# Performance work log

Hardware: AMD Instinct MI355X
Metric: run time of the kernel (lower is better)

## Reference

```python
import jax, jax.numpy as jnp
import numpy as np
from jax import lax

K = 3
PAD = 1
DIL = 1
BN_EPS = 1e-5


def setup_inputs() -> dict:
    key = jax.random.key(0)
    ks = jax.random.split(key, 7)
    B, C, O, H, W = 4, 64, 64, 128, 128
    x = jax.random.normal(ks[0], (B, C, H, W), jnp.float32)
    # offset conv params (zero-init in the module; small random here to exercise bilinear sampling)
    w_off = jax.random.normal(ks[1], (2 * K * K, C, K, K), jnp.float32) * 0.01
    b_off = jax.random.normal(ks[2], (2 * K * K,), jnp.float32) * 0.01
    # deformable conv params
    w_dcn = jax.random.normal(ks[3], (O, C, K, K), jnp.float32) / np.sqrt(C * K * K).astype(np.float32)
    b_dcn = jax.random.normal(ks[4], (O,), jnp.float32) * 0.01
    # BatchNorm affine params
    gamma = 1.0 + 0.1 * jax.random.normal(ks[5], (O,), jnp.float32)
    beta = 0.1 * jax.random.normal(ks[6], (O,), jnp.float32)
    return dict(x=x, w_off=w_off, b_off=b_off, w_dcn=w_dcn, b_dcn=b_dcn, gamma=gamma, beta=beta)


def _conv2d(x, w):
    return lax.conv_general_dilated(
        x, w, window_strides=(1, 1), padding=[(PAD, PAD), (PAD, PAD)],
        rhs_dilation=(DIL, DIL), dimension_numbers=('NCHW', 'OIHW', 'NCHW'))


def _gather(x, iy, ix):
    # x: [B,C,H,W]; iy/ix: [B,K2,H,W] int32 (already clipped in-range)
    B, C, H, W = x.shape
    idx = (iy * W + ix).reshape(B, -1)          # [B, K2*H*W]
    xf = x.reshape(B, C, H * W)
    v = jax.vmap(lambda xb, ib: xb[:, ib])(xf, idx)  # [B, C, K2*H*W]
    return v.reshape(B, C, iy.shape[1], H, W)


def _deform_sample(x, offset):
    # torchvision DeformConv2d v1: offsets are (dy, dx) pairs per kernel tap, zero-padding bilinear.
    B, C, H, W = x.shape
    K2 = K * K
    off = offset.reshape(B, K2, 2, H, W)
    ky = jnp.repeat(jnp.arange(K), K)   # tap row index, k = ky*K + kx
    kx = jnp.tile(jnp.arange(K), K)
    py = off[:, :, 0] + (ky * DIL - PAD)[None, :, None, None] + jnp.arange(H)[None, None, :, None]
    px = off[:, :, 1] + (kx * DIL - PAD)[None, :, None, None] + jnp.arange(W)[None, None, None, :]
    y0 = jnp.floor(py)
    x0 = jnp.floor(px)
    wy = py - y0
    wx = px - x0
    y0i = y0.astype(jnp.int32)
    x0i = x0.astype(jnp.int32)
    acc = jnp.zeros((B, C, K2, H, W), x.dtype)
    for dy, dx in ((0, 0), (0, 1), (1, 0), (1, 1)):
        iy = y0i + dy
        ix = x0i + dx
        wgt = (wy if dy else 1.0 - wy) * (wx if dx else 1.0 - wx)
        valid = (iy >= 0) & (iy < H) & (ix >= 0) & (ix < W)
        v = _gather(x, jnp.clip(iy, 0, H - 1), jnp.clip(ix, 0, W - 1))
        acc = acc + v * (wgt * valid.astype(x.dtype))[:, None]
    return acc  # [B, C, K2, H, W]


def reference(x, w_off, b_off, w_dcn, b_dcn, gamma, beta):
    offset = _conv2d(x, w_off) + b_off[None, :, None, None]
    patches = _deform_sample(x, offset)                     # [B,C,K2,H,W]
    O = w_dcn.shape[0]
    out = jnp.einsum('bckhw,ock->bohw', patches, w_dcn.reshape(O, -1, K * K))
    out = out + b_dcn[None, :, None, None]
    # BatchNorm2d in training mode: biased batch statistics over (B,H,W)
    mean = out.mean(axis=(0, 2, 3), keepdims=True)
    var = out.var(axis=(0, 2, 3), keepdims=True)
    out = (out - mean) * lax.rsqrt(var + BN_EPS)
    out = out * gamma[None, :, None, None] + beta[None, :, None, None]
    return jax.nn.relu(out)
```

## Files before the change

kernel.cpp:

```cpp
#include <hip/hip_runtime.h>

#define HW   16384
#define WID  128
#define HEI  128
#define CIN  64
#define OCH  64

typedef __attribute__((ext_vector_type(8))) short bf16x8;
typedef __attribute__((ext_vector_type(4))) short bf16x4;
typedef __attribute__((ext_vector_type(4))) float f32x4;

__device__ __forceinline__ unsigned short f2bf(float f) {
    unsigned u = __float_as_uint(f);
    u += 0x7FFF + ((u >> 16) & 1);
    return (unsigned short)(u >> 16);
}
__device__ __forceinline__ float bf2f(short s) {
    return __uint_as_float(((unsigned)(unsigned short)s) << 16);
}

__global__ __launch_bounds__(256) void kprep(const float* __restrict__ x,
                                             const float* __restrict__ wdcn,
                                             const float* __restrict__ woff,
                                             unsigned short* __restrict__ xt,
                                             unsigned short* __restrict__ wpack,
                                             unsigned short* __restrict__ woffpack) {
    int blk = blockIdx.x;
    if (blk < 256) {
        int gp = blk * 256 + threadIdx.x;
        int b = gp >> 14;
        int hw = gp & (HW - 1);
        const float* xb = x + (size_t)b * CIN * HW + hw;
        unsigned short* o = xt + ((size_t)gp << 6);
#pragma unroll
        for (int c8 = 0; c8 < 8; c8++) {
            bf16x8 v;
#pragma unroll
            for (int j = 0; j < 8; j++)
                v[j] = (short)f2bf(xb[(size_t)(c8 * 8 + j) * HW]);
            *(bf16x8*)(o + c8 * 8) = v;
        }
    } else {
        int t = (blk - 256) * 256 + threadIdx.x;
        if (t < 36864) {
            int j  = t & 7;
            int l  = (t >> 3) & 63;
            int nt = (t >> 9) & 3;
            int s  = t >> 11;
            int k  = s * 32 + (l >> 4) * 8 + j;
            int o  = nt * 16 + (l & 15);
            int tap = k >> 6, c = k & 63;
            wpack[t] = f2bf(wdcn[o * 576 + c * 9 + tap]);
        } else {
            int u  = t - 36864;
            int j  = u & 7;
            int l  = (u >> 3) & 63;
            int nt = (u >> 9) & 1;
            int s  = u >> 10;
            int k  = s * 32 + (l >> 4) * 8 + j;
            int o  = nt * 16 + (l & 15);
            int tap = k >> 6, c = k & 63;
            float v = (o < 18) ? woff[o * 576 + c * 9 + tap] : 0.f;
            woffpack[u] = f2bf(v);
        }
    }
}

__global__ __launch_bounds__(256, 4) void kdcn(const unsigned short* __restrict__ xt,
                                               const unsigned short* __restrict__ wpack,
                                               const unsigned short* __restrict__ woffpack,
                                               const float* __restrict__ boff,
                                               const float* __restrict__ bdcn,
                                               unsigned short* __restrict__ convb,
                                               float* __restrict__ part) {
    __shared__ __align__(16) unsigned char smem[39168];

    int tid = threadIdx.x;
    int lane = tid & 63, wave = tid >> 6;
    int lr = lane & 15, hi = lane >> 4;

    int pixg = blockIdx.x * 32;
    int b = pixg >> 14;
    int hwb = pixg & (HW - 1);
    int h = hwb >> 7;
    int w0 = hwb & (WID - 1);

    {
        int g = lane >> 3, sub = lane & 7;
        int px = wave * 8 + g;
        int w = w0 + px;
        const unsigned char* xtb =
            (const unsigned char*)xt + (((size_t)b * HW) << 7) + sub * 16;
        unsigned char* prow = smem + px * 1152;
        unsigned swz = (unsigned)((px & 7) << 4);
#pragma unroll
        for (int tap = 0; tap < 9; tap++) {
            int sy = h + tap / 3 - 1;
            int sx = w + tap % 3 - 1;
            bool ok = ((unsigned)sy < HEI) && ((unsigned)sx < WID);
            bf16x8 v = {0, 0, 0, 0, 0, 0, 0, 0};
            if (ok) v = *(const bf16x8*)(xtb + ((sy * WID + sx) << 7));
            *(bf16x8*)(prow + ((unsigned)(tap * 128 + sub * 16) ^ swz)) = v;
        }
    }
    __syncthreads();

    {
        int mw = wave & 1, nw = wave >> 1;
        int oc = nw * 16 + lr;
        float ob = (oc < 18) ? boff[oc] : 0.f;
        f32x4 oacc = {ob, ob, ob, ob};
        unsigned swzr = (unsigned)((lr & 7) << 4);
        const unsigned short* wop = woffpack + (size_t)(nw * 64 + lane) * 8;
        int arow = (mw * 16 + lr) * 1152;
#pragma unroll
        for (int s = 0; s < 18; s++) {
            unsigned inblk = (unsigned)((s >> 1) * 128)
                           + (((unsigned)((s & 1) * 64 + hi * 16)) ^ swzr);
            bf16x8 a  = *(const bf16x8*)(smem + arow + inblk);
            bf16x8 wf = *(const bf16x8*)(wop + (size_t)s * 1024);
            oacc = __builtin_amdgcn_mfma_f32_16x16x32_bf16(a, wf, oacc, 0, 0, 0);
        }
        float* offLds = (float*)(smem + 36864);
        if (oc < 18) {
#pragma unroll
            for (int r = 0; r < 4; r++)
                offLds[(mw * 16 + hi * 4 + r) * 18 + oc] = oacc[r];
        }
    }

    bf16x8 bfrag[18];
    const unsigned short* wp = wpack + (size_t)(wave * 64 + lane) * 8;
#pragma unroll
    for (int s = 0; s < 18; s++)
        bfrag[s] = *(const bf16x8*)(wp + (size_t)s * 2048);
    float bias = bdcn[wave * 16 + lr];
    __syncthreads();

    {
        int g = lane >> 3, sub = lane & 7;
        int px = wave * 8 + g;
        int w = w0 + px;
        const unsigned char* xtb =
            (const unsigned char*)xt + (((size_t)b * HW) << 7) + sub * 16;
        unsigned char* prow = smem + px * 1152;
        unsigned swz = (unsigned)((px & 7) << 4);
        const float* offL = (const float*)(smem + 36864) + px * 18;
#pragma unroll
        for (int tap = 0; tap < 9; tap++) {
            float dy = offL[tap * 2];
            float dx = offL[tap * 2 + 1];
            float py  = dy + (float)(h + tap / 3 - 1);
            float pxf = dx + (float)(w + tap % 3 - 1);
            float y0f = floorf(py), x0f = floorf(pxf);
            float wy = py - y0f, wx = pxf - x0f;
            int y0 = (int)y0f, x0 = (int)x0f;
            float wy0 = ((unsigned)y0       < HEI) ? 1.f - wy : 0.f;
            float wy1 = ((unsigned)(y0 + 1) < HEI) ? wy       : 0.f;
            float wx0 = ((unsigned)x0       < WID) ? 1.f - wx : 0.f;
            float wx1 = ((unsigned)(x0 + 1) < WID) ? wx       : 0.f;
            int yc0 = min(max(y0, 0),     HEI - 1) * WID;
            int yc1 = min(max(y0 + 1, 0), HEI - 1) * WID;
            int xc0 = min(max(x0, 0),     WID - 1);
            int xc1 = min(max(x0 + 1, 0), WID - 1);
            float w00 = wy0 * wx0, w01 = wy0 * wx1;
            float w10 = wy1 * wx0, w11 = wy1 * wx1;
            bf16x8 c00 = *(const bf16x8*)(xtb + ((yc0 + xc0) << 7));
            bf16x8 c01 = *(const bf16x8*)(xtb + ((yc0 + xc1) << 7));
            bf16x8 c10 = *(const bf16x8*)(xtb + ((yc1 + xc0) << 7));
            bf16x8 c11 = *(const bf16x8*)(xtb + ((yc1 + xc1) << 7));
            bf16x8 v;
#pragma unroll
            for (int j = 0; j < 8; j++) {
                float sv = w00 * bf2f(c00[j]) + w01 * bf2f(c01[j])
                         + w10 * bf2f(c10[j]) + w11 * bf2f(c11[j]);
                v[j] = (short)f2bf(sv);
            }
            *(bf16x8*)(prow + ((unsigned)(tap * 128 + sub * 16) ^ swz)) = v;
        }
    }
    __syncthreads();

    f32x4 acc0 = {bias, bias, bias, bias};
    f32x4 acc1 = acc0;
    unsigned swzr = (unsigned)((lr & 7) << 4);
#pragma unroll
    for (int s = 0; s < 18; s++) {
        unsigned inblk = (unsigned)((s >> 1) * 128)
                       + (((unsigned)((s & 1) * 64 + hi * 16)) ^ swzr);
        bf16x8 a0 = *(const bf16x8*)(smem + lr * 1152 + inblk);
        bf16x8 a1 = *(const bf16x8*)(smem + (16 + lr) * 1152 + inblk);
        acc0 = __builtin_amdgcn_mfma_f32_16x16x32_bf16(a0, bfrag[s], acc0, 0, 0, 0);
        acc1 = __builtin_amdgcn_mfma_f32_16x16x32_bf16(a1, bfrag[s], acc1, 0, 0, 0);
    }

    {
        int o = wave * 16 + lr;
        unsigned short* cb = convb + ((size_t)b * OCH + o) * HW + hwb + hi * 4;
        bf16x4 v0, v1;
#pragma unroll
        for (int r = 0; r < 4; r++) { v0[r] = (short)f2bf(acc0[r]);
                                      v1[r] = (short)f2bf(acc1[r]); }
        *(bf16x4*)cb        = v0;
        *(bf16x4*)(cb + 16) = v1;
    }

    {
        float s  = acc0[0] + acc0[1] + acc0[2] + acc0[3]
                 + acc1[0] + acc1[1] + acc1[2] + acc1[3];
        float s2 = acc0[0]*acc0[0] + acc0[1]*acc0[1] + acc0[2]*acc0[2] + acc0[3]*acc0[3]
                 + acc1[0]*acc1[0] + acc1[1]*acc1[1] + acc1[2]*acc1[2] + acc1[3]*acc1[3];
        s  += __shfl_xor(s, 16);  s2 += __shfl_xor(s2, 16);
        s  += __shfl_xor(s, 32);  s2 += __shfl_xor(s2, 32);
        if (hi == 0) {
            int c = wave * 16 + lr;
            part[(size_t)c * 2048 + blockIdx.x]        = s;
            part[(size_t)(64 + c) * 2048 + blockIdx.x] = s2;
        }
    }
}

__global__ __launch_bounds__(256) void kred(const float* __restrict__ part,
                                            float* __restrict__ stats) {
    int row = blockIdx.x;
    int tid = threadIdx.x;
    const float* p = part + (size_t)row * 2048;
    float s = 0.f;
#pragma unroll
    for (int i = 0; i < 8; i++) s += p[tid + i * 256];
#pragma unroll
    for (int d = 1; d < 64; d <<= 1) s += __shfl_xor(s, d);
    __shared__ float red[4];
    if ((tid & 63) == 0) red[tid >> 6] = s;
    __syncthreads();
    if (tid == 0) stats[row] = red[0] + red[1] + red[2] + red[3];
}

__global__ __launch_bounds__(256) void kapply(const unsigned short* __restrict__ convb,
                                              float* __restrict__ out,
                                              const float* __restrict__ stats,
                                              const float* __restrict__ gamma,
                                              const float* __restrict__ beta) {
    int t = blockIdx.x * 256 + threadIdx.x;
    int c = (t >> 12) & 63;
    float mean = stats[c] * (1.f / 65536.f);
    float var  = stats[64 + c] * (1.f / 65536.f) - mean * mean;
    float rstd = rsqrtf(var + 1e-5f);
    float sc = rstd * gamma[c];
    float sh = beta[c] - mean * sc;
    bf16x4 v = *(const bf16x4*)(convb + (size_t)t * 4);
    float4 r;
    r.x = fmaxf(bf2f(v[0]) * sc + sh, 0.f);
    r.y = fmaxf(bf2f(v[1]) * sc + sh, 0.f);
    r.z = fmaxf(bf2f(v[2]) * sc + sh, 0.f);
    r.w = fmaxf(bf2f(v[3]) * sc + sh, 0.f);
    ((float4*)out)[t] = r;
}

extern "C" void kernel_launch(void* const* d_in, const int* in_sizes, int n_in,
                              void* d_out, int out_size, void* d_ws, size_t ws_size,
                              hipStream_t stream) {
    const float* x     = (const float*)d_in[0];
    const float* woff  = (const float*)d_in[1];
    const float* boff  = (const float*)d_in[2];
    const float* wdcn  = (const float*)d_in[3];
    const float* bdcn  = (const float*)d_in[4];
    const float* gamma = (const float*)d_in[5];
    const float* beta  = (const float*)d_in[6];
    float* out = (float*)d_out;

    unsigned char* ws = (unsigned char*)d_ws;
    unsigned short* xt       = (unsigned short*)ws;
    unsigned short* wpack    = (unsigned short*)(ws + 8388608);
    unsigned short* woffpack = (unsigned short*)(ws + 8462336);
    float*          part     = (float*)(ws + 8499200);
    float*          stats    = (float*)(ws + 9547776);
    unsigned short* convb    = (unsigned short*)(ws + 9548288);

    hipLaunchKernelGGL(kprep,  dim3(472),  dim3(256), 0, stream,
                       x, wdcn, woff, xt, wpack, woffpack);
    hipLaunchKernelGGL(kdcn,   dim3(2048), dim3(256), 0, stream,
                       xt, wpack, woffpack, boff, bdcn, convb, part);
    hipLaunchKernelGGL(kred,   dim3(128),  dim3(256), 0, stream, part, stats);
    hipLaunchKernelGGL(kapply, dim3(4096), dim3(256), 0, stream,
                       convb, out, stats, gamma, beta);
}
```

Before: 56.62 us.

## Restructure deformable conv kernel so each wave independently owns 16 pixels

Each wave now processes 16 pixels on its own. A fragments are loaded straight from global memory into registers, so the shared-memory im2col staging and the block-wide barriers are gone. Each wave computes its own offset conv over two output tiles and all four DCN output-channel tiles, and streams B weights from global (L2) memory per step instead of holding them in registers. Per-wave partial sums double, so the reduction kernel reads 4096 entries per row. This trades LDS traffic and synchronisation for more global/L2 weight loads and less reuse of B fragments across pixels.

```diff
diff --git a/kernel.cpp b/kernel.cpp
--- a/kernel.cpp
+++ b/kernel.cpp
@@ -66,156 +66,135 @@
     }
 }
 
-__global__ __launch_bounds__(256, 4) void kdcn(const unsigned short* __restrict__ xt,
-                                               const unsigned short* __restrict__ wpack,
-                                               const unsigned short* __restrict__ woffpack,
-                                               const float* __restrict__ boff,
-                                               const float* __restrict__ bdcn,
-                                               unsigned short* __restrict__ convb,
-                                               float* __restrict__ part) {
-    __shared__ __align__(16) unsigned char smem[39168];
+__global__ __launch_bounds__(256) void kdcn(const unsigned short* __restrict__ xt,
+                                            const unsigned short* __restrict__ wpack,
+                                            const unsigned short* __restrict__ woffpack,
+                                            const float* __restrict__ boff,
+                                            const float* __restrict__ bdcn,
+                                            unsigned short* __restrict__ convb,
+                                            float* __restrict__ part) {
+    __shared__ float offLds[4][288];
 
     int tid = threadIdx.x;
     int lane = tid & 63, wave = tid >> 6;
     int lr = lane & 15, hi = lane >> 4;
 
-    int pixg = blockIdx.x * 32;
+    int gw = blockIdx.x * 4 + wave;
+    int pixg = gw << 4;
     int b = pixg >> 14;
     int hwb = pixg & (HW - 1);
     int h = hwb >> 7;
     int w0 = hwb & (WID - 1);
-
+    int px = lr;
+    int w = w0 + px;
+
+    const unsigned char* xtb =
+        (const unsigned char*)xt + (((size_t)b * HW) << 7) + hi * 16;
+
+    f32x4 oacc0, oacc1;
     {
-        int g = lane >> 3, sub = lane & 7;
-        int px = wave * 8 + g;
-        int w = w0 + px;
-        const unsigned char* xtb =
-            (const unsigned char*)xt + (((size_t)b * HW) << 7) + sub * 16;
-        unsigned char* prow = smem + px * 1152;
-        unsigned swz = (unsigned)((px & 7) << 4);
-#pragma unroll
-        for (int tap = 0; tap < 9; tap++) {
-            int sy = h + tap / 3 - 1;
-            int sx = w + tap % 3 - 1;
-            bool ok = ((unsigned)sy < HEI) && ((unsigned)sx < WID);
-            bf16x8 v = {0, 0, 0, 0, 0, 0, 0, 0};
-            if (ok) v = *(const bf16x8*)(xtb + ((sy * WID + sx) << 7));
-            *(bf16x8*)(prow + ((unsigned)(tap * 128 + sub * 16) ^ swz)) = v;
-        }
-    }
-    __syncthreads();
-
-    {
-        int mw = wave & 1, nw = wave >> 1;
-        int oc = nw * 16 + lr;
-        float ob = (oc < 18) ? boff[oc] : 0.f;
-        f32x4 oacc = {ob, ob, ob, ob};
-        unsigned swzr = (unsigned)((lr & 7) << 4);
-        const unsigned short* wop = woffpack + (size_t)(nw * 64 + lane) * 8;
-        int arow = (mw * 16 + lr) * 1152;
-#pragma unroll
-        for (int s = 0; s < 18; s++) {
-            unsigned inblk = (unsigned)((s >> 1) * 128)
-                           + (((unsigned)((s & 1) * 64 + hi * 16)) ^ swzr);
-            bf16x8 a  = *(const bf16x8*)(smem + arow + inblk);
-            bf16x8 wf = *(const bf16x8*)(wop + (size_t)s * 1024);
-            oacc = __builtin_amdgcn_mfma_f32_16x16x32_bf16(a, wf, oacc, 0, 0, 0);
-        }
-        float* offLds = (float*)(smem + 36864);
-        if (oc < 18) {
-#pragma unroll
-            for (int r = 0; r < 4; r++)
-                offLds[(mw * 16 + hi * 4 + r) * 18 + oc] = oacc[r];
-        }
-    }
-
-    bf16x8 bfrag[18];
-    const unsigned short* wp = wpack + (size_t)(wave * 64 + lane) * 8;
-#pragma unroll
-    for (int s = 0; s < 18; s++)
-        bfrag[s] = *(const bf16x8*)(wp + (size_t)s * 2048);
-    float bias = bdcn[wave * 16 + lr];
-    __syncthreads();
-
-    {
-        int g = lane >> 3, sub = lane & 7;
-        int px = wave * 8 + g;
-        int w = w0 + px;
-        const unsigned char* xtb =
-            (const unsigned char*)xt + (((size_t)b * HW) << 7) + sub * 16;
-        unsigned char* prow = smem + px * 1152;
-        unsigned swz = (unsigned)((px & 7) << 4);
-        const float* offL = (const float*)(smem + 36864) + px * 18;
-#pragma unroll
-        for (int tap = 0; tap < 9; tap++) {
-            float dy = offL[tap * 2];
-            float dx = offL[tap * 2 + 1];
-            float py  = dy + (float)(h + tap / 3 - 1);
-            float pxf = dx + (float)(w + tap % 3 - 1);
-            float y0f = floorf(py), x0f = floorf(pxf);
-            float wy = py - y0f, wx = pxf - x0f;
-            int y0 = (int)y0f, x0 = (int)x0f;
-            float wy0 = ((unsigned)y0       < HEI) ? 1.f - wy : 0.f;
-            float wy1 = ((unsigned)(y0 + 1) < HEI) ? wy       : 0.f;
-            float wx0 = ((unsigned)x0       < WID) ? 1.f - wx : 0.f;
-            float wx1 = ((unsigned)(x0 + 1) < WID) ? wx       : 0.f;
-            int yc0 = min(max(y0, 0),     HEI - 1) * WID;
-            int yc1 = min(max(y0 + 1, 0), HEI - 1) * WID;
-            int xc0 = min(max(x0, 0),     WID - 1);
-            int xc1 = min(max(x0 + 1, 0), WID - 1);
-            float w00 = wy0 * wx0, w01 = wy0 * wx1;
-            float w10 = wy1 * wx0, w11 = wy1 * wx1;
-            bf16x8 c00 = *(const bf16x8*)(xtb + ((yc0 + xc0) << 7));
-            bf16x8 c01 = *(const bf16x8*)(xtb + ((yc0 + xc1) << 7));
-            bf16x8 c10 = *(const bf16x8*)(xtb + ((yc1 + xc0) << 7));
-            bf16x8 c11 = *(const bf16x8*)(xtb + ((yc1 + xc1) << 7));
-            bf16x8 v;
-#pragma unroll
-            for (int j = 0; j < 8; j++) {
-                float sv = w00 * bf2f(c00[j]) + w01 * bf2f(c01[j])
-                         + w10 * bf2f(c10[j]) + w11 * bf2f(c11[j]);
-                v[j] = (short)f2bf(sv);
-            }
-            *(bf16x8*)(prow + ((unsigned)(tap * 128 + sub * 16) ^ swz)) = v;
-        }
-    }
-    __syncthreads();
-
-    f32x4 acc0 = {bias, bias, bias, bias};
-    f32x4 acc1 = acc0;
-    unsigned swzr = (unsigned)((lr & 7) << 4);
+        float ob0 = boff[lr];
+        float ob1 = (lr < 2) ? boff[16 + lr] : 0.f;
+        oacc0 = f32x4{ob0, ob0, ob0, ob0};
+        oacc1 = f32x4{ob1, ob1, ob1, ob1};
+    }
 #pragma unroll
     for (int s = 0; s < 18; s++) {
-        unsigned inblk = (unsigned)((s >> 1) * 128)
-                       + (((unsigned)((s & 1) * 64 + hi * 16)) ^ swzr);
-        bf16x8 a0 = *(const bf16x8*)(smem + lr * 1152 + inblk);
-        bf16x8 a1 = *(const bf16x8*)(smem + (16 + lr) * 1152 + inblk);
-        acc0 = __builtin_amdgcn_mfma_f32_16x16x32_bf16(a0, bfrag[s], acc0, 0, 0, 0);
-        acc1 = __builtin_amdgcn_mfma_f32_16x16x32_bf16(a1, bfrag[s], acc1, 0, 0, 0);
-    }
-
-    {
-        int o = wave * 16 + lr;
+        int tap = s >> 1;
+        int sy = h + tap / 3 - 1;
+        int sx = w + tap % 3 - 1;
+        bool ok = ((unsigned)sy < HEI) && ((unsigned)sx < WID);
+        bf16x8 a = {0, 0, 0, 0, 0, 0, 0, 0};
+        if (ok) a = *(const bf16x8*)(xtb + ((sy * WID + sx) << 7) + (s & 1) * 64);
+        bf16x8 b0 = *(const bf16x8*)(woffpack + s * 1024 + lane * 8);
+        bf16x8 b1 = *(const bf16x8*)(woffpack + s * 1024 + 512 + lane * 8);
+        oacc0 = __builtin_amdgcn_mfma_f32_16x16x32_bf16(a, b0, oacc0, 0, 0, 0);
+        oacc1 = __builtin_amdgcn_mfma_f32_16x16x32_bf16(a, b1, oacc1, 0, 0, 0);
+    }
+    float* oL = offLds[wave];
+#pragma unroll
+    for (int r = 0; r < 4; r++) {
+        oL[(hi * 4 + r) * 18 + lr] = oacc0[r];
+        if (lr < 2) oL[(hi * 4 + r) * 18 + 16 + lr] = oacc1[r];
+    }
+
+    f32x4 acc[4];
+#pragma unroll
+    for (int nt = 0; nt < 4; nt++) {
+        float bv = bdcn[nt * 16 + lr];
+        acc[nt] = f32x4{bv, bv, bv, bv};
+    }
+
+#pragma unroll
+    for (int tap = 0; tap < 9; tap++) {
+        float dy = oL[px * 18 + 2 * tap];
+        float dx = oL[px * 18 + 2 * tap + 1];
+        float py  = dy + (float)(h + tap / 3 - 1);
+        float pxf = dx + (float)(w + tap % 3 - 1);
+        float y0f = floorf(py), x0f = floorf(pxf);
+        float wy = py - y0f, wx = pxf - x0f;
+        int y0 = (int)y0f, x0 = (int)x0f;
+        float wy0 = ((unsigned)y0       < HEI) ? 1.f - wy : 0.f;
+        float wy1 = ((unsigned)(y0 + 1) < HEI) ? wy       : 0.f;
+        float wx0 = ((unsigned)x0       < WID) ? 1.f - wx : 0.f;
+        float wx1 = ((unsigned)(x0 + 1) < WID) ? wx       : 0.f;
+        int yc0 = min(max(y0, 0),     HEI - 1) * WID;
+        int yc1 = min(max(y0 + 1, 0), HEI - 1) * WID;
+        int xc0 = min(max(x0, 0),     WID - 1);
+        int xc1 = min(max(x0 + 1, 0), WID - 1);
+        float w00 = wy0 * wx0, w01 = wy0 * wx1;
+        float w10 = wy1 * wx0, w11 = wy1 * wx1;
+        int b00 = (yc0 + xc0) << 7, b01 = (yc0 + xc1) << 7;
+        int b10 = (yc1 + xc0) << 7, b11 = (yc1 + xc1) << 7;
+        bf16x8 c00a = *(const bf16x8*)(xtb + b00);
+        bf16x8 c01a = *(const bf16x8*)(xtb + b01);
+        bf16x8 c10a = *(const bf16x8*)(xtb + b10);
+        bf16x8 c11a = *(const bf16x8*)(xtb + b11);
+        bf16x8 c00b = *(const bf16x8*)(xtb + b00 + 64);
+        bf16x8 c01b = *(const bf16x8*)(xtb + b01 + 64);
+        bf16x8 c10b = *(const bf16x8*)(xtb + b10 + 64);
+        bf16x8 c11b = *(const bf16x8*)(xtb + b11 + 64);
+        bf16x8 a0, a1;
+#pragma unroll
+        for (int j = 0; j < 8; j++) {
+            float sa = w00 * bf2f(c00a[j]) + w01 * bf2f(c01a[j])
+                     + w10 * bf2f(c10a[j]) + w11 * bf2f(c11a[j]);
+            float sb = w00 * bf2f(c00b[j]) + w01 * bf2f(c01b[j])
+                     + w10 * bf2f(c10b[j]) + w11 * bf2f(c11b[j]);
+            a0[j] = (short)f2bf(sa);
+            a1[j] = (short)f2bf(sb);
+        }
+        int s0 = 2 * tap, s1 = 2 * tap + 1;
+#pragma unroll
+        for (int nt = 0; nt < 4; nt++) {
+            bf16x8 bf0 = *(const bf16x8*)(wpack + s0 * 2048 + nt * 512 + lane * 8);
+            bf16x8 bf1 = *(const bf16x8*)(wpack + s1 * 2048 + nt * 512 + lane * 8);
+            acc[nt] = __builtin_amdgcn_mfma_f32_16x16x32_bf16(a0, bf0, acc[nt], 0, 0, 0);
+            acc[nt] = __builtin_amdgcn_mfma_f32_16x16x32_bf16(a1, bf1, acc[nt], 0, 0, 0);
+        }
+    }
+
+#pragma unroll
+    for (int nt = 0; nt < 4; nt++) {
+        int o = nt * 16 + lr;
         unsigned short* cb = convb + ((size_t)b * OCH + o) * HW + hwb + hi * 4;
-        bf16x4 v0, v1;
-#pragma unroll
-        for (int r = 0; r < 4; r++) { v0[r] = (short)f2bf(acc0[r]);
-                                      v1[r] = (short)f2bf(acc1[r]); }
-        *(bf16x4*)cb        = v0;
-        *(bf16x4*)(cb + 16) = v1;
-    }
-
-    {
-        float s  = acc0[0] + acc0[1] + acc0[2] + acc0[3]
-                 + acc1[0] + acc1[1] + acc1[2] + acc1[3];
-        float s2 = acc0[0]*acc0[0] + acc0[1]*acc0[1] + acc0[2]*acc0[2] + acc0[3]*acc0[3]
-                 + acc1[0]*acc1[0] + acc1[1]*acc1[1] + acc1[2]*acc1[2] + acc1[3]*acc1[3];
+        bf16x4 v;
+#pragma unroll
+        for (int r = 0; r < 4; r++) v[r] = (short)f2bf(acc[nt][r]);
+        *(bf16x4*)cb = v;
+    }
+
+#pragma unroll
+    for (int nt = 0; nt < 4; nt++) {
+        float s  = acc[nt][0] + acc[nt][1] + acc[nt][2] + acc[nt][3];
+        float s2 = acc[nt][0]*acc[nt][0] + acc[nt][1]*acc[nt][1]
+                 + acc[nt][2]*acc[nt][2] + acc[nt][3]*acc[nt][3];
         s  += __shfl_xor(s, 16);  s2 += __shfl_xor(s2, 16);
         s  += __shfl_xor(s, 32);  s2 += __shfl_xor(s2, 32);
         if (hi == 0) {
-            int c = wave * 16 + lr;
-            part[(size_t)c * 2048 + blockIdx.x]        = s;
-            part[(size_t)(64 + c) * 2048 + blockIdx.x] = s2;
+            int c = nt * 16 + lr;
+            part[(size_t)c * 4096 + gw]        = s;
+            part[(size_t)(64 + c) * 4096 + gw] = s2;
         }
     }
 }
@@ -224,10 +203,10 @@
                                             float* __restrict__ stats) {
     int row = blockIdx.x;
     int tid = threadIdx.x;
-    const float* p = part + (size_t)row * 2048;
+    const float* p = part + (size_t)row * 4096;
     float s = 0.f;
 #pragma unroll
-    for (int i = 0; i < 8; i++) s += p[tid + i * 256];
+    for (int i = 0; i < 16; i++) s += p[tid + i * 256];
 #pragma unroll
     for (int d = 1; d < 64; d <<= 1) s += __shfl_xor(s, d);
     __shared__ float red[4];
@@ -274,12 +253,12 @@
     unsigned short* wpack    = (unsigned short*)(ws + 8388608);
     unsigned short* woffpack = (unsigned short*)(ws + 8462336);
     float*          part     = (float*)(ws + 8499200);
-    float*          stats    = (float*)(ws + 9547776);
-    unsigned short* convb    = (unsigned short*)(ws + 9548288);
+    float*          stats    = (float*)(ws + 10596352);
+    unsigned short* convb    = (unsigned short*)(ws + 10596864);
 
     hipLaunchKernelGGL(kprep,  dim3(472),  dim3(256), 0, stream,
                        x, wdcn, woff, xt, wpack, woffpack);
-    hipLaunchKernelGGL(kdcn,   dim3(2048), dim3(256), 0, stream,
+    hipLaunchKernelGGL(kdcn,   dim3(1024), dim3(256), 0, stream,
                        xt, wpack, woffpack, boff, bdcn, convb, part);
     hipLaunchKernelGGL(kred,   dim3(128),  dim3(256), 0, stream, part, stats);
     hipLaunchKernelGGL(kapply, dim3(4096), dim3(256), 0, stream,
```

New measurement: 76.03 us. +34.3%, slower.
